# Kernel optimization log

Hardware: AMD Instinct MI355X
Metric: run time of the kernel (lower is better)

Reference implementation:

```python
import jax, jax.numpy as jnp
import numpy as np

N_NODES = 100000
N_EDGES = 1200000
IN_CH = 128
HID = 256
OUT_CH = 64
N_ETYPES = 8
N_DIFF = 1000


def setup_inputs() -> dict:
    key = jax.random.key(0)
    ks = jax.random.split(key, 20)
    s = 0.05
    inp = {
        'x': jax.random.normal(ks[0], (N_NODES, IN_CH), jnp.float32),
        'edge_index': jax.random.randint(ks[1], (2, N_EDGES), 0, N_NODES, jnp.int64),
        'edge_type': jax.random.randint(ks[2], (N_EDGES,), 0, N_ETYPES, jnp.int64),
        'diff_idx': jax.random.randint(ks[3], (N_DIFF,), 0, N_NODES, jnp.int64),
        # lin: in_ch -> hid -> out_ch
        'lin1_w': jax.random.normal(ks[4], (HID, IN_CH), jnp.float32) * s,
        'lin1_b': jnp.zeros((HID,), jnp.float32),
        'lin2_w': jax.random.normal(ks[5], (OUT_CH, HID), jnp.float32) * s,
        'lin2_b': jnp.zeros((OUT_CH,), jnp.float32),
        # GRUCell(out_ch, out_ch): gates ordered r, z, n as in torch
        'gru_w_ih': jax.random.normal(ks[6], (3 * OUT_CH, OUT_CH), jnp.float32) * s,
        'gru_w_hh': jax.random.normal(ks[7], (3 * OUT_CH, OUT_CH), jnp.float32) * s,
        'gru_b_ih': jnp.zeros((3 * OUT_CH,), jnp.float32),
        'gru_b_hh': jnp.zeros((3 * OUT_CH,), jnp.float32),
        'edge_type_weight': jax.random.normal(ks[8], (N_ETYPES,), jnp.float32),
        # fc: out_ch -> hid -> 2
        'fc1_w': jax.random.normal(ks[9], (HID, OUT_CH), jnp.float32) * s,
        'fc1_b': jnp.zeros((HID,), jnp.float32),
        'fc2_w': jax.random.normal(ks[10], (2, HID), jnp.float32) * s,
        'fc2_b': jnp.zeros((2,), jnp.float32),
        'w_imp': jnp.float32(1.0),
    }
    return inp


def _gru_cell(m, h, w_ih, w_hh, b_ih, b_hh):
    # torch GRUCell: gates [r, z, n]
    gi = m @ w_ih.T + b_ih  # [N, 3H]
    gh = h @ w_hh.T + b_hh
    gi_r, gi_z, gi_n = jnp.split(gi, 3, axis=-1)
    gh_r, gh_z, gh_n = jnp.split(gh, 3, axis=-1)
    r = jax.nn.sigmoid(gi_r + gh_r)
    z = jax.nn.sigmoid(gi_z + gh_z)
    n = jnp.tanh(gi_n + r * gh_n)
    return (1.0 - z) * n + z * h


def reference(x, edge_index, edge_type, diff_idx,
              lin1_w, lin1_b, lin2_w, lin2_b,
              gru_w_ih, gru_w_hh, gru_b_ih, gru_b_hh,
              edge_type_weight,
              fc1_w, fc1_b, fc2_w, fc2_b, w_imp):
    N = x.shape[0]
    src, dst = edge_index[0], edge_index[1]
    # input projection MLP
    h = jax.nn.relu(x @ lin1_w.T + lin1_b) @ lin2_w.T + lin2_b  # [N, OUT]
    # per-edge softplus weight (constant across iterations)
    w_e = jax.nn.softplus(edge_type_weight[edge_type])[:, None]  # [E, 1]
    # degree for mean aggregation (isolated nodes -> 0 message)
    deg = jax.ops.segment_sum(jnp.ones_like(src, dtype=h.dtype), dst, num_segments=N)
    deg = jnp.maximum(deg, 1.0)[:, None]
    for _ in range(3):
        msg = w_e * h[src]  # gather + weight, [E, OUT]
        m = jax.ops.segment_sum(msg, dst, num_segments=N) / deg  # scatter-mean
        h = _gru_cell(m, h, gru_w_ih, gru_w_hh, gru_b_ih, gru_b_hh)
    # importance-weighted global pooling
    w_pos = jax.nn.softplus(w_imp)
    alpha = jnp.ones((N, 1), h.dtype).at[diff_idx].set(1.0 + w_pos)
    pooled = (alpha * h).sum(axis=0, keepdims=True) / alpha.sum()  # [1, OUT]
    out = jax.nn.relu(pooled @ fc1_w.T + fc1_b) @ fc2_w.T + fc2_b  # [1, 2]
    return jax.nn.log_softmax(out, axis=1)
```

## Files before the change

### kernel.cpp

```cpp
#include <hip/hip_runtime.h>
#include <math.h>

#define NN 100000
#define NE 1200000
#define NDIFF 1000
#define CAP 48
#define SLICE 2048
#define NQ 200
#define SUBN 500
#define QCAPB 32
#define NSH 8
#define SQS 1024
#define NSPLAY 32
#define PSTRIDE 132
#define NGEMM 1563
#define NBIN 586

typedef short short8 __attribute__((ext_vector_type(8)));
typedef float floatx4 __attribute__((ext_vector_type(4)));
typedef float floatx2 __attribute__((ext_vector_type(2)));
typedef int intx4 __attribute__((ext_vector_type(4)));
typedef unsigned short ushort_t;
typedef unsigned long long ull_t;

__device__ __forceinline__ float softplusf_(float x) {
  return fmaxf(x, 0.f) + logf(1.f + __expf(-fabsf(x)));
}
__device__ __forceinline__ float sigmoidf_(float x) {
  return 1.f / (1.f + __expf(-x));
}
__device__ __forceinline__ float tanhf_fast(float x) {
  float ax = fabsf(x);
  float e = __expf(-2.f * ax);
  float t = (1.f - e) / (1.f + e);
  return x < 0.f ? -t : t;
}
__device__ __forceinline__ ushort_t f2bf(float f) {
  unsigned u = __float_as_uint(f);
  unsigned r = (u + 0x7FFFu + ((u >> 16) & 1u)) >> 16;
  return (ushort_t)r;
}
__device__ __forceinline__ float bf2f(ushort_t s) {
  return __uint_as_float(((unsigned)s) << 16);
}
__device__ __forceinline__ uint2 bf8_to_fp8x8(short8 v) {
  float f[8];
  #pragma unroll
  for (int i = 0; i < 8; ++i) f[i] = bf2f((ushort_t)v[i]);
  int a = 0, b = 0;
  a = __builtin_amdgcn_cvt_pk_fp8_f32(f[0], f[1], a, false);
  a = __builtin_amdgcn_cvt_pk_fp8_f32(f[2], f[3], a, true);
  b = __builtin_amdgcn_cvt_pk_fp8_f32(f[4], f[5], b, false);
  b = __builtin_amdgcn_cvt_pk_fp8_f32(f[6], f[7], b, true);
  uint2 r; r.x = (unsigned)a; r.y = (unsigned)b;
  return r;
}


__global__ void prep_w_kernel(const float* __restrict__ lin1_w, const float* __restrict__ lin2_w,
                              const float* __restrict__ w_ih, const float* __restrict__ w_hh,
                              const float* __restrict__ etw, const int* __restrict__ diff,
                              ushort_t* __restrict__ W1s, ushort_t* __restrict__ W2s,
                              ushort_t* __restrict__ Wcs, float* __restrict__ wtab,
                              unsigned char* __restrict__ flagb) {
  int i = blockIdx.x * 256 + threadIdx.x;
  if (i < 8) wtab[i] = softplusf_(etw[i]);
  if (i < NDIFF) flagb[diff[i]] = 1;
  if (i < 32768) {
    int fi = i >> 9, lane = (i >> 3) & 63, j = i & 7;
    int s = fi >> 4, ct = fi & 15;
    int quad = lane >> 4, l15 = lane & 15;
    int col = ct * 16 + l15, k = s * 32 + quad * 8 + j;
    W1s[i] = f2bf(lin1_w[col * 128 + k]);
  } else if (i < 49152) {
    int i2 = i - 32768;
    int fi = i2 >> 9, lane = (i2 >> 3) & 63, j = i2 & 7;
    int s = fi >> 2, ct = fi & 3;
    int quad = lane >> 4, l15 = lane & 15;
    int col = ct * 16 + l15, k = s * 32 + quad * 8 + j;
    W2s[i2] = f2bf(lin2_w[col * 256 + k]);
  } else {
    int i3 = i - 49152;
    int fi = i3 >> 9, lane = (i3 >> 3) & 63, j = i3 & 7;
    int s = fi >> 4, ct = fi & 15;
    int quad = lane >> 4, l15 = lane & 15;
    int jj = ct * 16 + l15, k = s * 32 + quad * 8 + j;
    float v;
    if (jj < 128)      v = (k < 64) ? w_ih[jj * 64 + k] : w_hh[jj * 64 + (k - 64)];
    else if (jj < 192) v = (k < 64) ? w_ih[jj * 64 + k] : 0.f;
    else               v = (k < 64) ? 0.f : w_hh[(jj - 64) * 64 + (k - 64)];
    Wcs[i3] = f2bf(v);
  }
}


__launch_bounds__(256)
__global__ void binmlp_kernel(const float* __restrict__ x,
                              const ushort_t* __restrict__ W1s, const float* __restrict__ b1,
                              const ushort_t* __restrict__ W2s, const float* __restrict__ b2,
                              ushort_t* __restrict__ mh, unsigned char* __restrict__ h8,
                              const int* __restrict__ src, const int* __restrict__ dst,
                              const int* __restrict__ etype,
                              unsigned* __restrict__ gtail, unsigned* __restrict__ staging) {
  __shared__ __align__(16) char U[33792];
  int t = threadIdx.x;

  if (blockIdx.x < NGEMM) {
    ushort_t* S = (ushort_t*)U;
    int wv = t >> 6, lane = t & 63;
    int quad = lane >> 4, l15 = lane & 15;
    int nb = blockIdx.x * 64;

    #pragma unroll
    for (int it = 0; it < 8; ++it) {
      int f = it * 256 + t;
      int row = f >> 5, off4 = f & 31;
      int grow = min(nb + row, NN - 1);
      float4 v = *(const float4*)&x[(size_t)grow * 128 + off4 * 4];
      union { uint2 d; ushort_t u[4]; } pk;
      pk.u[0] = f2bf(v.x); pk.u[1] = f2bf(v.y); pk.u[2] = f2bf(v.z); pk.u[3] = f2bf(v.w);
      *(uint2*)&S[row * 136 + off4 * 4] = pk.d;
    }
    __syncthreads();

    floatx4 acc1[4][4];
    #pragma unroll
    for (int rt = 0; rt < 4; ++rt)
      #pragma unroll
      for (int c = 0; c < 4; ++c) acc1[rt][c] = (floatx4)0.f;

    #pragma unroll
    for (int s = 0; s < 4; ++s) {
      short8 av[4];
      #pragma unroll
      for (int rt = 0; rt < 4; ++rt)
        av[rt] = *(const short8*)&S[(rt * 16 + l15) * 136 + s * 32 + quad * 8];
      #pragma unroll
      for (int c = 0; c < 4; ++c) {
        short8 bv = *(const short8*)&W1s[((s * 16 + wv * 4 + c) * 64 + lane) * 8];
        #pragma unroll
        for (int rt = 0; rt < 4; ++rt)
          acc1[rt][c] = __builtin_amdgcn_mfma_f32_16x16x32_bf16(av[rt], bv, acc1[rt][c], 0, 0, 0);
      }
    }
    __syncthreads();

    #pragma unroll
    for (int c = 0; c < 4; ++c) {
      int col = (wv * 4 + c) * 16 + l15;
      float bb = b1[col];
      #pragma unroll
      for (int rt = 0; rt < 4; ++rt)
        #pragma unroll
        for (int reg = 0; reg < 4; ++reg)
          S[(rt * 16 + quad * 4 + reg) * 264 + col] = f2bf(fmaxf(acc1[rt][c][reg] + bb, 0.f));
    }
    __syncthreads();

    floatx4 acc2[4];
    #pragma unroll
    for (int c = 0; c < 4; ++c) acc2[c] = (floatx4)0.f;
    #pragma unroll
    for (int s = 0; s < 8; ++s) {
      short8 av = *(const short8*)&S[(wv * 16 + l15) * 264 + s * 32 + quad * 8];
      #pragma unroll
      for (int c = 0; c < 4; ++c) {
        short8 bv = *(const short8*)&W2s[((s * 4 + c) * 64 + lane) * 8];
        acc2[c] = __builtin_amdgcn_mfma_f32_16x16x32_bf16(av, bv, acc2[c], 0, 0, 0);
      }
    }
    __syncthreads();

    #pragma unroll
    for (int c = 0; c < 4; ++c) {
      int col = c * 16 + l15;
      float bb = b2[c * 16 + l15];
      #pragma unroll
      for (int reg = 0; reg < 4; ++reg)
        S[(wv * 16 + quad * 4 + reg) * 72 + col] = f2bf(acc2[c][reg] + bb);
    }
    __syncthreads();

    #pragma unroll
    for (int it = 0; it < 2; ++it) {
      int idx = it * 256 + t;
      int row = idx >> 3, ch = idx & 7;
      int node = nb + row;
      if (node < NN) {
        short8 v = *(const short8*)&S[row * 72 + ch * 8];
        *(short8*)&mh[(size_t)node * 64 + ch * 8] = v;
        *(uint2*)&h8[(size_t)node * 64 + ch * 8] = bf8_to_fp8x8(v);
      }
    }
  } else {
    unsigned (*bin)[QCAPB] = (unsigned (*)[QCAPB])U;
    unsigned* lcur = (unsigned*)(U + NQ * QCAPB * 4);
    int bid = blockIdx.x - NGEMM;
    int shard = bid & 7;
    for (int i = t; i < NQ; i += 256) lcur[i] = 0;
    __syncthreads();
    int base = bid * SLICE;

    unsigned rec[8];
    int qq[8];
    unsigned idx[8];
    #pragma unroll
    for (int it = 0; it < 8; ++it) {
      int e = base + it * 256 + t;
      qq[it] = -1;
      if (e < NE) {
        int d = __builtin_nontemporal_load(&dst[e]);
        int s = __builtin_nontemporal_load(&src[e]);
        int tv = __builtin_nontemporal_load(&etype[e]);
        int q = d / SUBN;
        int local = d - q * SUBN;
        rec[it] = ((unsigned)local << 20) | (unsigned)(s | (tv << 17));
        qq[it] = q;
        unsigned i = atomicAdd(&lcur[q], 1u);
        idx[it] = i;
        if (i < QCAPB) bin[q][i] = rec[it];
      }
    }
    __syncthreads();
    if (t < NQ) {
      unsigned c = min(lcur[t], (unsigned)QCAPB);
      if (c) {
        unsigned gb = atomicAdd(&gtail[(t * NSH + shard) * 16], c);
        unsigned* qst = staging + (size_t)(t * NSH + shard) * SQS + gb;
        const unsigned* b = bin[t];
        for (unsigned i = 0; i < c; ++i) qst[i] = b[i];
      }
    }
    #pragma unroll
    for (int it = 0; it < 8; ++it) {
      if (qq[it] >= 0 && idx[it] >= QCAPB) {
        unsigned gb = atomicAdd(&gtail[(qq[it] * NSH + shard) * 16], 1u);
        staging[(size_t)(qq[it] * NSH + shard) * SQS + gb] = rec[it];
      }
    }
  }
}


__launch_bounds__(512)
__global__ void scatter_kernel(const unsigned* __restrict__ staging,
                               const unsigned* __restrict__ gtail,
                               unsigned* __restrict__ cpack, int* __restrict__ csr) {
  __shared__ int cnt[SUBN];
  int t = threadIdx.x;
  int q = blockIdx.x;
  int n0 = q * SUBN;
  for (int i = t; i < SUBN; i += 512) cnt[i] = 0;
  __syncthreads();

  #pragma unroll 1
  for (int sh = 0; sh < NSH; ++sh) {
    unsigned n = gtail[(q * NSH + sh) * 16];
    const unsigned* st = staging + (size_t)(q * NSH + sh) * SQS;
    for (unsigned i = t; i < n; i += 512) {
      unsigned r = st[i];
      int local = r >> 20;
      int rank = atomicAdd(&cnt[local], 1);
      csr[(n0 + local) * CAP + rank] = (int)(r & 0xFFFFF);
    }
  }
  __syncthreads();

  if (t < SUBN / 4) {
    unsigned w = (unsigned)cnt[t * 4] | ((unsigned)cnt[t * 4 + 1] << 8) |
                 ((unsigned)cnt[t * 4 + 2] << 16) | ((unsigned)cnt[t * 4 + 3] << 24);
    cpack[(n0 >> 2) + t] = w;
  }
}


template <bool LAST>
__launch_bounds__(256, 8)
__global__ void agru_kernel(const ushort_t* __restrict__ mhin,
                            const unsigned char* __restrict__ h8in,
                            const unsigned* __restrict__ cpack,
                            const int* __restrict__ csr, const float* __restrict__ wtab,
                            const ushort_t* __restrict__ Wcs,
                            const float* __restrict__ b_ih, const float* __restrict__ b_hh,
                            ushort_t* __restrict__ mhout, unsigned char* __restrict__ h8out,
                            const unsigned char* __restrict__ flagb,
                            float* __restrict__ pooled) {
  __shared__ ushort_t As[32 * 136];
  __shared__ ushort_t Os[32 * 72];
  __shared__ float wt[16];
  __shared__ float red[132];
  int t = threadIdx.x;
  int nb = blockIdx.x * 32;
  if (t < 16) wt[t] = (t < 8) ? wtab[t] : 0.f;
  if (LAST) { for (int i = t; i < 132; i += 256) red[i] = 0.f; }
  __syncthreads();

  int g8 = t >> 3, lane8 = t & 7;
  int node = nb + g8;

  short8 hreg = *(const short8*)&mhin[(size_t)node * 64 + lane8 * 8];

  int deg = (cpack[node >> 2] >> ((node & 3) * 8)) & 255;
  const intx4* crow = (const intx4*)(csr + (size_t)node * CAP);
  float f0 = 0.f, f1 = 0.f, f2 = 0.f, f3 = 0.f;
  float f4 = 0.f, f5 = 0.f, f6 = 0.f, f7 = 0.f;
  for (int p = 0; p < deg; p += 12) {
    intx4 k4[3];
    #pragma unroll
    for (int c = 0; c < 3; ++c)
      k4[c] = __builtin_nontemporal_load(&crow[(p >> 2) + c]);
    int k[12];
    #pragma unroll
    for (int c = 0; c < 3; ++c) {
      k[c * 4 + 0] = k4[c][0]; k[c * 4 + 1] = k4[c][1];
      k[c * 4 + 2] = k4[c][2]; k[c * 4 + 3] = k4[c][3];
    }
    #pragma unroll
    for (int i = 0; i < 12; ++i)
      if (p + i >= deg) k[i] = (8 << 17);
    uint2 v[12];
    #pragma unroll
    for (int i = 0; i < 12; ++i)
      v[i] = *(const uint2*)&h8in[(size_t)(k[i] & 0x1FFFF) * 64 + lane8 * 8];
    #pragma unroll
    for (int i = 0; i < 12; ++i) {
      float w = wt[k[i] >> 17];
      floatx2 xlo = __builtin_amdgcn_cvt_pk_f32_fp8((int)v[i].x, false);
      floatx2 xhi = __builtin_amdgcn_cvt_pk_f32_fp8((int)v[i].x, true);
      floatx2 ylo = __builtin_amdgcn_cvt_pk_f32_fp8((int)v[i].y, false);
      floatx2 yhi = __builtin_amdgcn_cvt_pk_f32_fp8((int)v[i].y, true);
      f0 += w * xlo[0]; f1 += w * xlo[1]; f2 += w * xhi[0]; f3 += w * xhi[1];
      f4 += w * ylo[0]; f5 += w * ylo[1]; f6 += w * yhi[0]; f7 += w * yhi[1];
    }
  }
  {
    float invd = 1.f / fmaxf((float)deg, 1.f);
    short8 pk;
    pk[0] = (short)f2bf(f0 * invd); pk[1] = (short)f2bf(f1 * invd);
    pk[2] = (short)f2bf(f2 * invd); pk[3] = (short)f2bf(f3 * invd);
    pk[4] = (short)f2bf(f4 * invd); pk[5] = (short)f2bf(f5 * invd);
    pk[6] = (short)f2bf(f6 * invd); pk[7] = (short)f2bf(f7 * invd);
    *(short8*)&As[g8 * 136 + lane8 * 8] = pk;
    *(short8*)&As[g8 * 136 + 64 + lane8 * 8] = hreg;
  }
  __syncthreads();

  int wv = t >> 6, lane = t & 63;
  int quad = lane >> 4, l15 = lane & 15;

  floatx4 acc[2][4];
  #pragma unroll
  for (int rt = 0; rt < 2; ++rt)
    #pragma unroll
    for (int g = 0; g < 4; ++g) acc[rt][g] = (floatx4)0.f;

  #pragma unroll
  for (int s4 = 0; s4 < 4; ++s4) {
    short8 av[2];
    #pragma unroll
    for (int rt = 0; rt < 2; ++rt)
      av[rt] = *(const short8*)&As[(rt * 16 + l15) * 136 + s4 * 32 + quad * 8];
    #pragma unroll
    for (int g = 0; g < 4; ++g) {
      short8 bv = *(const short8*)&Wcs[((s4 * 16 + g * 4 + wv) * 64 + lane) * 8];
      #pragma unroll
      for (int rt = 0; rt < 2; ++rt)
        acc[rt][g] = __builtin_amdgcn_mfma_f32_16x16x32_bf16(av[rt], bv, acc[rt][g], 0, 0, 0);
    }
  }

  int j = wv * 16 + l15;
  float bir = b_ih[j] + b_hh[j];
  float biz = b_ih[64 + j] + b_hh[64 + j];
  float bin_ = b_ih[128 + j];
  float bhn = b_hh[128 + j];

  if (!LAST) {
    #pragma unroll
    for (int rt = 0; rt < 2; ++rt) {
      #pragma unroll
      for (int reg = 0; reg < 4; ++reg) {
        int lrow = rt * 16 + quad * 4 + reg;
        float r = sigmoidf_(acc[rt][0][reg] + bir);
        float z = sigmoidf_(acc[rt][1][reg] + biz);
        float n = tanhf_fast(acc[rt][2][reg] + bin_ + r * (acc[rt][3][reg] + bhn));
        float hp = bf2f(As[lrow * 136 + 64 + j]);
        Os[lrow * 72 + j] = f2bf((1.f - z) * n + z * hp);
      }
    }
    __syncthreads();
    short8 vo = *(const short8*)&Os[g8 * 72 + lane8 * 8];
    *(short8*)&mhout[(size_t)node * 64 + lane8 * 8] = vo;
    *(uint2*)&h8out[(size_t)node * 64 + lane8 * 8] = bf8_to_fp8x8(vo);
  } else {
    float psum = 0.f, fsum = 0.f;
    #pragma unroll
    for (int rt = 0; rt < 2; ++rt) {
      #pragma unroll
      for (int reg = 0; reg < 4; ++reg) {
        int lrow = rt * 16 + quad * 4 + reg;
        float r = sigmoidf_(acc[rt][0][reg] + bir);
        float z = sigmoidf_(acc[rt][1][reg] + biz);
        float n = tanhf_fast(acc[rt][2][reg] + bin_ + r * (acc[rt][3][reg] + bhn));
        float hp = bf2f(As[lrow * 136 + 64 + j]);
        float hn = (1.f - z) * n + z * hp;
        psum += hn;
        if (flagb[nb + lrow]) fsum += hn;
      }
    }
    atomicAdd(&red[j], psum);
    atomicAdd(&red[64 + j], fsum);
    if (t < 32) { if (flagb[nb + t]) atomicAdd(&red[128], 1.f); }
    __syncthreads();
    if (t < 129) atomicAdd(&pooled[(blockIdx.x & (NSPLAY - 1)) * PSTRIDE + t], red[t]);
  }
}


__global__ void final_kernel(const float* __restrict__ pooled,
                             const float* __restrict__ fc1_w, const float* __restrict__ fc1_b,
                             const float* __restrict__ fc2_w, const float* __restrict__ fc2_b,
                             const float* __restrict__ w_imp, float* __restrict__ out) {
  __shared__ float p[64];
  __shared__ float hid[256];
  __shared__ float o[2];
  __shared__ float cnt_s;
  int t = threadIdx.x;
  float wpos = softplusf_(w_imp[0]);
  float b = 0.f, f = 0.f;
  if (t < 64) {
    #pragma unroll 4
    for (int k = 0; k < NSPLAY; ++k) {
      b += pooled[k * PSTRIDE + t];
      f += pooled[k * PSTRIDE + 64 + t];
    }
  }
  if (t == 64) {
    float c = 0.f;
    for (int k = 0; k < NSPLAY; ++k) c += pooled[k * PSTRIDE + 128];
    cnt_s = c;
  }
  __syncthreads();
  if (t < 64) {
    float den = (float)NN + wpos * cnt_s;
    p[t] = (b + wpos * f) / den;
  }
  __syncthreads();
  {
    float a = 0.f;
    for (int k = 0; k < 64; ++k) a += p[k] * fc1_w[t * 64 + k];
    hid[t] = fmaxf(a + fc1_b[t], 0.f);
  }
  __syncthreads();
  if (t < 2) {
    float a = 0.f;
    for (int k = 0; k < 256; ++k) a += hid[k] * fc2_w[t * 256 + k];
    o[t] = a + fc2_b[t];
  }
  __syncthreads();
  if (t == 0) {
    float mx = fmaxf(o[0], o[1]);
    float lse = mx + logf(__expf(o[0] - mx) + __expf(o[1] - mx));
    out[0] = o[0] - lse;
    out[1] = o[1] - lse;
  }
}


extern "C" void kernel_launch(void* const* d_in, const int* in_sizes, int n_in,
                              void* d_out, int out_size, void* d_ws, size_t ws_size,
                              hipStream_t stream) {
  const float* x        = (const float*)d_in[0];
  const int*   ei       = (const int*)d_in[1];
  const int*   etype    = (const int*)d_in[2];
  const int*   diff_idx = (const int*)d_in[3];
  const float* lin1_w   = (const float*)d_in[4];
  const float* lin1_b   = (const float*)d_in[5];
  const float* lin2_w   = (const float*)d_in[6];
  const float* lin2_b   = (const float*)d_in[7];
  const float* gru_w_ih = (const float*)d_in[8];
  const float* gru_w_hh = (const float*)d_in[9];
  const float* gru_b_ih = (const float*)d_in[10];
  const float* gru_b_hh = (const float*)d_in[11];
  const float* etw      = (const float*)d_in[12];
  const float* fc1_w    = (const float*)d_in[13];
  const float* fc1_b    = (const float*)d_in[14];
  const float* fc2_w    = (const float*)d_in[15];
  const float* fc2_b    = (const float*)d_in[16];
  const float* w_imp    = (const float*)d_in[17];
  float* out = (float*)d_out;

  char* ws = (char*)d_ws;
  size_t off = 0;
  auto alloc = [&](size_t bytes) -> void* {
    void* p = ws + off;
    off += (bytes + 255) & ~(size_t)255;
    return p;
  };
  ushort_t* mh0   = (ushort_t*)alloc((size_t)NN * 64 * 2);
  ushort_t* mh1   = (ushort_t*)alloc((size_t)NN * 64 * 2);
  unsigned char* h8a = (unsigned char*)alloc((size_t)NN * 64);
  unsigned char* h8b = (unsigned char*)alloc((size_t)NN * 64);
  int*   csr      = (int*)  alloc((size_t)NN * CAP * 4 + 64);
  unsigned* staging = (unsigned*)alloc((size_t)NQ * NSH * SQS * 4);
  ushort_t* W1s   = (ushort_t*)alloc(128 * 256 * 2);
  ushort_t* W2s   = (ushort_t*)alloc(256 * 64 * 2);
  ushort_t* Wcs   = (ushort_t*)alloc(128 * 256 * 2);
  float* wtab     = (float*)alloc(8 * 4);
  const size_t gtb = (size_t)NQ * NSH * 16 * 4;
  const size_t plb = (size_t)NSPLAY * PSTRIDE * 4;
  char* zbase     = (char*)alloc(gtb + (size_t)NN + NN + plb);
  unsigned* gtail = (unsigned*)zbase;
  unsigned* cpack = (unsigned*)(zbase + gtb);
  unsigned char* flagb = (unsigned char*)(zbase + gtb + NN);
  float* pooled   = (float*)(zbase + gtb + NN + NN);
  const size_t zbytes = gtb + (size_t)NN + NN + plb;

  const int nagru = NN / 32;

  (void)hipMemsetAsync(zbase, 0, zbytes, stream);
  prep_w_kernel<<<320, 256, 0, stream>>>(lin1_w, lin2_w, gru_w_ih, gru_w_hh, etw, diff_idx,
                                         W1s, W2s, Wcs, wtab, flagb);
  binmlp_kernel<<<NGEMM + NBIN, 256, 0, stream>>>(x, W1s, lin1_b, W2s, lin2_b, mh0, h8a,
                                                  ei, ei + NE, etype, gtail, staging);
  scatter_kernel<<<NQ, 512, 0, stream>>>(staging, gtail, cpack, csr);

  agru_kernel<false><<<nagru, 256, 0, stream>>>(mh0, h8a, cpack, csr, wtab, Wcs,
                                                gru_b_ih, gru_b_hh, mh1, h8b, flagb, pooled);
  agru_kernel<false><<<nagru, 256, 0, stream>>>(mh1, h8b, cpack, csr, wtab, Wcs,
                                                gru_b_ih, gru_b_hh, mh0, h8a, flagb, pooled);
  agru_kernel<true><<<nagru, 256, 0, stream>>>(mh0, h8a, cpack, csr, wtab, Wcs,
                                               gru_b_ih, gru_b_hh, mh1, h8b, flagb, pooled);

  final_kernel<<<1, 256, 0, stream>>>(pooled, fc1_w, fc1_b, fc2_w, fc2_b, w_imp, out);
}
```

Measured before the change: 293.5 us.

## Fold memset into prep kernel, pre-shift CSR offsets, pad CSR rows, pack accumulators

Removes the hipMemsetAsync by zeroing the counters, flags and pooled buffers inside prep_w_kernel, and moves diff-flag setting into scatter_kernel so it runs after the zeroing. The CSR now stores the byte offset (node*64) with the edge type in the high bits, and each row is padded to a multiple of 12 with a zero-weight sentinel. This drops the per-element bounds check and the address multiply in the aggregation loop. Accumulation uses packed float2 FMAs. The scatter kernel gains padding writes and the prep grid grows.

Result: slower. 309.2 us (+5.4%).

```diff
diff --git a/kernel.cpp b/kernel.cpp
--- a/kernel.cpp
+++ b/kernel.cpp
@@ -59,13 +59,16 @@
 
 __global__ void prep_w_kernel(const float* __restrict__ lin1_w, const float* __restrict__ lin2_w,
                               const float* __restrict__ w_ih, const float* __restrict__ w_hh,
-                              const float* __restrict__ etw, const int* __restrict__ diff,
+                              const float* __restrict__ etw,
                               ushort_t* __restrict__ W1s, ushort_t* __restrict__ W2s,
                               ushort_t* __restrict__ Wcs, float* __restrict__ wtab,
-                              unsigned char* __restrict__ flagb) {
+                              unsigned* __restrict__ flag4, unsigned* __restrict__ gtail,
+                              float* __restrict__ pooled) {
   int i = blockIdx.x * 256 + threadIdx.x;
   if (i < 8) wtab[i] = softplusf_(etw[i]);
-  if (i < NDIFF) flagb[diff[i]] = 1;
+  if (i < NN / 4) flag4[i] = 0;
+  if (i < NQ * NSH * 16) gtail[i] = 0;
+  if (i < NSPLAY * PSTRIDE) pooled[i] = 0.f;
   if (i < 32768) {
     int fi = i >> 9, lane = (i >> 3) & 63, j = i & 7;
     int s = fi >> 4, ct = fi & 15;
@@ -79,7 +82,7 @@
     int quad = lane >> 4, l15 = lane & 15;
     int col = ct * 16 + l15, k = s * 32 + quad * 8 + j;
     W2s[i2] = f2bf(lin2_w[col * 256 + k]);
-  } else {
+  } else if (i < 81920) {
     int i3 = i - 49152;
     int fi = i3 >> 9, lane = (i3 >> 3) & 63, j = i3 & 7;
     int s = fi >> 4, ct = fi & 15;
@@ -245,11 +248,16 @@
 __launch_bounds__(512)
 __global__ void scatter_kernel(const unsigned* __restrict__ staging,
                                const unsigned* __restrict__ gtail,
-                               unsigned* __restrict__ cpack, int* __restrict__ csr) {
+                               unsigned* __restrict__ cpack, int* __restrict__ csr,
+                               const int* __restrict__ diff, unsigned char* __restrict__ flagb) {
   __shared__ int cnt[SUBN];
   int t = threadIdx.x;
   int q = blockIdx.x;
   int n0 = q * SUBN;
+  {
+    int di = q * 512 + t;
+    if (di < NDIFF) flagb[diff[di]] = 1;
+  }
   for (int i = t; i < SUBN; i += 512) cnt[i] = 0;
   __syncthreads();
 
@@ -261,11 +269,18 @@
       unsigned r = st[i];
       int local = r >> 20;
       int rank = atomicAdd(&cnt[local], 1);
-      csr[(n0 + local) * CAP + rank] = (int)(r & 0xFFFFF);
-    }
-  }
-  __syncthreads();
-
+      csr[(n0 + local) * CAP + rank] =
+          (int)((((r >> 17) & 7u) << 23) | ((r & 0x1FFFFu) << 6));
+    }
+  }
+  __syncthreads();
+
+  for (int i = t; i < SUBN; i += 512) {
+    int dg = cnt[i];
+    int pe = ((dg + 11) / 12) * 12;
+    for (int s2 = dg; s2 < pe; ++s2)
+      csr[(n0 + i) * CAP + s2] = (int)(8u << 23);
+  }
   if (t < SUBN / 4) {
     unsigned w = (unsigned)cnt[t * 4] | ((unsigned)cnt[t * 4 + 1] << 8) |
                  ((unsigned)cnt[t * 4 + 2] << 16) | ((unsigned)cnt[t * 4 + 3] << 24);
@@ -302,44 +317,40 @@
 
   int deg = (cpack[node >> 2] >> ((node & 3) * 8)) & 255;
   const intx4* crow = (const intx4*)(csr + (size_t)node * CAP);
-  float f0 = 0.f, f1 = 0.f, f2 = 0.f, f3 = 0.f;
-  float f4 = 0.f, f5 = 0.f, f6 = 0.f, f7 = 0.f;
+  const unsigned char* h8l = h8in + lane8 * 8;
+  floatx2 a0 = {0.f, 0.f}, a1 = {0.f, 0.f}, a2 = {0.f, 0.f}, a3 = {0.f, 0.f};
   for (int p = 0; p < deg; p += 12) {
     intx4 k4[3];
     #pragma unroll
     for (int c = 0; c < 3; ++c)
       k4[c] = __builtin_nontemporal_load(&crow[(p >> 2) + c]);
-    int k[12];
+    unsigned k[12];
     #pragma unroll
     for (int c = 0; c < 3; ++c) {
-      k[c * 4 + 0] = k4[c][0]; k[c * 4 + 1] = k4[c][1];
-      k[c * 4 + 2] = k4[c][2]; k[c * 4 + 3] = k4[c][3];
-    }
+      k[c * 4 + 0] = (unsigned)k4[c][0]; k[c * 4 + 1] = (unsigned)k4[c][1];
+      k[c * 4 + 2] = (unsigned)k4[c][2]; k[c * 4 + 3] = (unsigned)k4[c][3];
+    }
+    uint2 v[12];
     #pragma unroll
     for (int i = 0; i < 12; ++i)
-      if (p + i >= deg) k[i] = (8 << 17);
-    uint2 v[12];
-    #pragma unroll
-    for (int i = 0; i < 12; ++i)
-      v[i] = *(const uint2*)&h8in[(size_t)(k[i] & 0x1FFFF) * 64 + lane8 * 8];
+      v[i] = *(const uint2*)&h8l[k[i] & 0x7FFFC0u];
     #pragma unroll
     for (int i = 0; i < 12; ++i) {
-      float w = wt[k[i] >> 17];
-      floatx2 xlo = __builtin_amdgcn_cvt_pk_f32_fp8((int)v[i].x, false);
-      floatx2 xhi = __builtin_amdgcn_cvt_pk_f32_fp8((int)v[i].x, true);
-      floatx2 ylo = __builtin_amdgcn_cvt_pk_f32_fp8((int)v[i].y, false);
-      floatx2 yhi = __builtin_amdgcn_cvt_pk_f32_fp8((int)v[i].y, true);
-      f0 += w * xlo[0]; f1 += w * xlo[1]; f2 += w * xhi[0]; f3 += w * xhi[1];
-      f4 += w * ylo[0]; f5 += w * ylo[1]; f6 += w * yhi[0]; f7 += w * yhi[1];
+      float w = wt[k[i] >> 23];
+      floatx2 w2 = {w, w};
+      a0 += w2 * __builtin_amdgcn_cvt_pk_f32_fp8((int)v[i].x, false);
+      a1 += w2 * __builtin_amdgcn_cvt_pk_f32_fp8((int)v[i].x, true);
+      a2 += w2 * __builtin_amdgcn_cvt_pk_f32_fp8((int)v[i].y, false);
+      a3 += w2 * __builtin_amdgcn_cvt_pk_f32_fp8((int)v[i].y, true);
     }
   }
   {
     float invd = 1.f / fmaxf((float)deg, 1.f);
     short8 pk;
-    pk[0] = (short)f2bf(f0 * invd); pk[1] = (short)f2bf(f1 * invd);
-    pk[2] = (short)f2bf(f2 * invd); pk[3] = (short)f2bf(f3 * invd);
-    pk[4] = (short)f2bf(f4 * invd); pk[5] = (short)f2bf(f5 * invd);
-    pk[6] = (short)f2bf(f6 * invd); pk[7] = (short)f2bf(f7 * invd);
+    pk[0] = (short)f2bf(a0[0] * invd); pk[1] = (short)f2bf(a0[1] * invd);
+    pk[2] = (short)f2bf(a1[0] * invd); pk[3] = (short)f2bf(a1[1] * invd);
+    pk[4] = (short)f2bf(a2[0] * invd); pk[5] = (short)f2bf(a2[1] * invd);
+    pk[6] = (short)f2bf(a3[0] * invd); pk[7] = (short)f2bf(a3[1] * invd);
     *(short8*)&As[g8 * 136 + lane8 * 8] = pk;
     *(short8*)&As[g8 * 136 + 64 + lane8 * 8] = hreg;
   }
@@ -509,21 +520,20 @@
   float* wtab     = (float*)alloc(8 * 4);
   const size_t gtb = (size_t)NQ * NSH * 16 * 4;
   const size_t plb = (size_t)NSPLAY * PSTRIDE * 4;
-  char* zbase     = (char*)alloc(gtb + (size_t)NN + NN + plb);
+  char* zbase     = (char*)alloc(gtb + (size_t)NN + plb);
   unsigned* gtail = (unsigned*)zbase;
-  unsigned* cpack = (unsigned*)(zbase + gtb);
-  unsigned char* flagb = (unsigned char*)(zbase + gtb + NN);
-  float* pooled   = (float*)(zbase + gtb + NN + NN);
-  const size_t zbytes = gtb + (size_t)NN + NN + plb;
+  unsigned char* flagb = (unsigned char*)(zbase + gtb);
+  float* pooled   = (float*)(zbase + gtb + NN);
+  unsigned* cpack = (unsigned*)alloc((size_t)NN);
 
   const int nagru = NN / 32;
 
-  (void)hipMemsetAsync(zbase, 0, zbytes, stream);
-  prep_w_kernel<<<320, 256, 0, stream>>>(lin1_w, lin2_w, gru_w_ih, gru_w_hh, etw, diff_idx,
-                                         W1s, W2s, Wcs, wtab, flagb);
+  prep_w_kernel<<<400, 256, 0, stream>>>(lin1_w, lin2_w, gru_w_ih, gru_w_hh, etw,
+                                         W1s, W2s, Wcs, wtab,
+                                         (unsigned*)flagb, gtail, pooled);
   binmlp_kernel<<<NGEMM + NBIN, 256, 0, stream>>>(x, W1s, lin1_b, W2s, lin2_b, mh0, h8a,
                                                   ei, ei + NE, etype, gtail, staging);
-  scatter_kernel<<<NQ, 512, 0, stream>>>(staging, gtail, cpack, csr);
+  scatter_kernel<<<NQ, 512, 0, stream>>>(staging, gtail, cpack, csr, diff_idx, flagb);
 
   agru_kernel<false><<<nagru, 256, 0, stream>>>(mh0, h8a, cpack, csr, wtab, Wcs,
                                                 gru_b_ih, gru_b_hh, mh1, h8b, flagb, pooled);
```
